# Optimization experiments

Measured on AMD Instinct MI355X. Metric: run time of the kernel, lower is better.

The kernel has to match this reference:

```python
import jax, jax.numpy as jnp
import numpy as np

NQ = 4          # number of qubits (hardcoded in the original module)
LET = 'pqrs'    # einsum letters for the 4 qubit axes


def setup_inputs() -> dict:
    key = jax.random.key(0)
    k1, k2 = jax.random.split(key)
    B = 1048576  # 2^20 samples
    x = jax.random.normal(k1, (B, NQ), dtype=jnp.float32)          # RX angles per sample
    weights = jax.random.normal(k2, (3, NQ, 3), dtype=jnp.float32) * 0.1  # (layers, wires, 3)
    return {"x": x, "weights": weights}


def _apply_1q(state, U, w):
    # state: (B,2,2,2,2) complex, U: (2,2) complex, applied on wire w
    sub = 'b' + LET
    out = sub.replace(LET[w], 'x')
    return jnp.einsum(f'x{LET[w]},{sub}->{out}', U, state)


def _cnot(state, c, t):
    # CNOT control c -> target t: flip target axis on the control=1 half
    s0, s1 = jnp.split(state, 2, axis=1 + c)
    s1 = jnp.flip(s1, axis=1 + t)
    return jnp.concatenate([s0, s1], axis=1 + c)


def _rot(phi, theta, omega):
    # PennyLane Rot(phi, theta, omega) = RZ(omega) RY(theta) RZ(phi)
    c = jnp.cos(theta * 0.5)
    s = jnp.sin(theta * 0.5)
    m00 = jnp.exp(-0.5j * (phi + omega)) * c
    m01 = -jnp.exp(0.5j * (phi - omega)) * s
    m10 = jnp.exp(-0.5j * (phi - omega)) * s
    m11 = jnp.exp(0.5j * (phi + omega)) * c
    return jnp.stack([jnp.stack([m00, m01]), jnp.stack([m10, m11])]).astype(jnp.complex64)


def _forward(x, weights):
    # --- RX(x_i) on |0>^4: product state, built as an outer product ---
    c = jnp.cos(x * 0.5)
    s = jnp.sin(x * 0.5)
    mi = np.complex64(-1j)
    vs = [jnp.stack([c[:, i].astype(jnp.complex64), mi * s[:, i]], axis=-1) for i in range(NQ)]
    state = jnp.einsum('bp,bq,br,bs->bpqrs', *vs)  # (B,2,2,2,2) complex64

    # --- StronglyEntanglingLayers (default ranges r = l % (NQ-1) + 1) ---
    n_layers = weights.shape[0]
    for l in range(n_layers):
        for i in range(NQ):
            U = _rot(weights[l, i, 0], weights[l, i, 1], weights[l, i, 2])
            state = _apply_1q(state, U, i)
        r = (l % (NQ - 1)) + 1
        for i in range(NQ):
            state = _cnot(state, i, (i + r) % NQ)

    # --- <Z_i> expectation values ---
    probs = state.real ** 2 + state.imag ** 2  # (B,2,2,2,2) float32
    outs = []
    for w in range(NQ):
        axes = tuple(a for a in range(1, NQ + 1) if a != w + 1)
        m = probs.sum(axis=axes)  # (B,2) marginal over wire w
        outs.append(m[:, 0] - m[:, 1])
    return jnp.stack(outs, axis=-1)  # (B, NQ)


def reference(x, weights):
    return _forward(x, weights)
```

## Files before the change

kernel.cpp:

```cpp
#include <hip/hip_runtime.h>
#include <hip/hip_bf16.h>


__global__ void build_V_kernel(const float* __restrict__ w, float* __restrict__ V) {
    int k = threadIdx.x;
    if (k >= 16) return;

    float ar[16], ai[16];
#pragma unroll
    for (int j = 0; j < 16; ++j) { ar[j] = (j == k) ? 1.f : 0.f; ai[j] = 0.f; }

#pragma unroll
    for (int l = 0; l < 3; ++l) {
#pragma unroll
        for (int i = 0; i < 4; ++i) {
            float phi = w[l * 12 + i * 3 + 0];
            float th  = w[l * 12 + i * 3 + 1];
            float om  = w[l * 12 + i * 3 + 2];
            float ct = cosf(0.5f * th), st = sinf(0.5f * th);
            float alpha = 0.5f * (phi + om), beta = 0.5f * (phi - om);
            float sa, ca, sb, cb;
            sincosf(alpha, &sa, &ca);
            sincosf(beta,  &sb, &cb);
            float m00r =  ca * ct, m00i = -sa * ct;
            float m01r = -cb * st, m01i = -sb * st;
            float m10r =  cb * st, m10i = -sb * st;
            float m11r =  ca * ct, m11i =  sa * ct;
            int mask = 1 << i;
#pragma unroll
            for (int j = 0; j < 16; ++j) {
                if (j & mask) continue;
                int j1 = j | mask;
                float a0r = ar[j],  a0i = ai[j];
                float a1r = ar[j1], a1i = ai[j1];
                ar[j]  = m00r * a0r - m00i * a0i + m01r * a1r - m01i * a1i;
                ai[j]  = m00r * a0i + m00i * a0r + m01r * a1i + m01i * a1r;
                ar[j1] = m10r * a0r - m10i * a0i + m11r * a1r - m11i * a1i;
                ai[j1] = m10r * a0i + m10i * a0r + m11r * a1i + m11i * a1r;
            }
        }
        int r = (l % 3) + 1;
#pragma unroll
        for (int i = 0; i < 4; ++i) {
            int c = i, t = (i + r) & 3;
            int cm = 1 << c, tm = 1 << t;
#pragma unroll
            for (int j = 0; j < 16; ++j) {
                if ((j & cm) && !(j & tm)) {
                    int j2 = j | tm;
                    float tr = ar[j], ti = ai[j];
                    ar[j] = ar[j2]; ai[j] = ai[j2];
                    ar[j2] = tr;    ai[j2] = ti;
                }
            }
        }
    }

    int p = __popc(k) & 3;
    float pr = (p == 0) ? 1.f : (p == 2) ? -1.f : 0.f;
    float pi = (p == 1) ? -1.f : (p == 3) ? 1.f : 0.f;
#pragma unroll
    for (int j = 0; j < 16; ++j) {
        float vr = ar[j] * pr - ai[j] * pi;
        float vi = ar[j] * pi + ai[j] * pr;
        V[j * 32 + k]      = vr;
        V[j * 32 + 16 + k] = vi;
    }
}

#define SAMPLES_PER_THREAD 2
#define BLOCK 256

__launch_bounds__(BLOCK)
__global__ void qlayer_kernel(const float* __restrict__ x,
                              const float* __restrict__ Vg,
                              float* __restrict__ out, int B) {
    __shared__ float V[512];
    {
        int t = threadIdx.x;
        if (t < 128) ((float4*)V)[t] = ((const float4*)Vg)[t];
    }
    __syncthreads();

    int base = blockIdx.x * (BLOCK * SAMPLES_PER_THREAD) + threadIdx.x;

#pragma unroll
    for (int s = 0; s < SAMPLES_PER_THREAD; ++s) {
        int idx = base + s * BLOCK;
        if (idx < B) {
            float4 xv = ((const float4*)x)[idx];
            float c0, s0, c1, s1, c2, s2, c3, s3;
            __sincosf(0.5f * xv.x, &s0, &c0);
            __sincosf(0.5f * xv.y, &s1, &c1);
            __sincosf(0.5f * xv.z, &s2, &c2);
            __sincosf(0.5f * xv.w, &s3, &c3);

            float m[16];
            m[0] = c0; m[1] = s0;
            m[2] = m[0] * s1; m[3] = m[1] * s1;
            m[0] *= c1;       m[1] *= c1;
#pragma unroll
            for (int k = 0; k < 4; ++k) { m[4 + k] = m[k] * s2; m[k] *= c2; }
#pragma unroll
            for (int k = 0; k < 8; ++k) { m[8 + k] = m[k] * s3; m[k] *= c3; }

            float z0 = 0.f, z1 = 0.f, z2 = 0.f, z3 = 0.f;
#pragma unroll
            for (int j = 0; j < 16; ++j) {
                float re = 0.f, im = 0.f;
#pragma unroll
                for (int k = 0; k < 16; ++k) {
                    re = fmaf(V[j * 32 + k],      m[k], re);
                    im = fmaf(V[j * 32 + 16 + k], m[k], im);
                }
                float p = fmaf(re, re, im * im);
                z0 += (j & 1) ? -p : p;
                z1 += (j & 2) ? -p : p;
                z2 += (j & 4) ? -p : p;
                z3 += (j & 8) ? -p : p;
            }
            float4 o; o.x = z0; o.y = z1; o.z = z2; o.w = z3;
            ((float4*)out)[idx] = o;
        }
    }
}

extern "C" void kernel_launch(void* const* d_in, const int* in_sizes, int n_in,
                              void* d_out, int out_size, void* d_ws, size_t ws_size,
                              hipStream_t stream) {
    const float* x = (const float*)d_in[0];
    const float* w = (const float*)d_in[1];
    float* out = (float*)d_out;
    float* V = (float*)d_ws;

    int B = in_sizes[0] / 4;

    build_V_kernel<<<1, 64, 0, stream>>>(w, V);

    int samples_per_block = BLOCK * SAMPLES_PER_THREAD;
    int grid = (B + samples_per_block - 1) / samples_per_block;
    qlayer_kernel<<<grid, BLOCK, 0, stream>>>(x, V, out, B);
}
```

Measured before the change: 97.74 us.

## Read V matrix from global/scalar path and reuse each coefficient across four samples

Drops the shared-memory staging of the 16x16 complex V matrix and reads it straight from global memory. V indices are uniform across the wavefront, so these loads can go through scalar loads. The loop is reordered so each V element is loaded once and applied to four samples per thread, and a template removes bounds checks when B divides evenly. This cuts LDS traffic and load count per FMA, at the cost of more VGPRs (64 mask values plus accumulators), which may lower occupancy.

```diff
diff --git a/kernel.cpp b/kernel.cpp
--- a/kernel.cpp
+++ b/kernel.cpp
@@ -68,58 +68,73 @@
     }
 }
 
-#define SAMPLES_PER_THREAD 2
+#define SPT 4
 #define BLOCK 256
 
+template <bool GUARD>
 __launch_bounds__(BLOCK)
 __global__ void qlayer_kernel(const float* __restrict__ x,
-                              const float* __restrict__ Vg,
+                              const float* __restrict__ V,
                               float* __restrict__ out, int B) {
-    __shared__ float V[512];
-    {
-        int t = threadIdx.x;
-        if (t < 128) ((float4*)V)[t] = ((const float4*)Vg)[t];
-    }
-    __syncthreads();
+    const int base = blockIdx.x * (BLOCK * SPT) + threadIdx.x;
 
-    int base = blockIdx.x * (BLOCK * SAMPLES_PER_THREAD) + threadIdx.x;
+    float m[SPT][16];
+    float z[SPT][4];
 
 #pragma unroll
-    for (int s = 0; s < SAMPLES_PER_THREAD; ++s) {
+    for (int s = 0; s < SPT; ++s) {
         int idx = base + s * BLOCK;
-        if (idx < B) {
-            float4 xv = ((const float4*)x)[idx];
-            float c0, s0, c1, s1, c2, s2, c3, s3;
-            __sincosf(0.5f * xv.x, &s0, &c0);
-            __sincosf(0.5f * xv.y, &s1, &c1);
-            __sincosf(0.5f * xv.z, &s2, &c2);
-            __sincosf(0.5f * xv.w, &s3, &c3);
+        float4 xv;
+        if (!GUARD || idx < B) xv = ((const float4*)x)[idx];
+        else xv = make_float4(0.f, 0.f, 0.f, 0.f);
+        float c0, s0, c1, s1, c2, s2, c3, s3;
+        __sincosf(0.5f * xv.x, &s0, &c0);
+        __sincosf(0.5f * xv.y, &s1, &c1);
+        __sincosf(0.5f * xv.z, &s2, &c2);
+        __sincosf(0.5f * xv.w, &s3, &c3);
 
-            float m[16];
-            m[0] = c0; m[1] = s0;
-            m[2] = m[0] * s1; m[3] = m[1] * s1;
-            m[0] *= c1;       m[1] *= c1;
+        float* ms = m[s];
+        ms[0] = c0; ms[1] = s0;
+        ms[2] = ms[0] * s1; ms[3] = ms[1] * s1;
+        ms[0] *= c1;        ms[1] *= c1;
 #pragma unroll
-            for (int k = 0; k < 4; ++k) { m[4 + k] = m[k] * s2; m[k] *= c2; }
+        for (int k = 0; k < 4; ++k) { ms[4 + k] = ms[k] * s2; ms[k] *= c2; }
 #pragma unroll
-            for (int k = 0; k < 8; ++k) { m[8 + k] = m[k] * s3; m[k] *= c3; }
+        for (int k = 0; k < 8; ++k) { ms[8 + k] = ms[k] * s3; ms[k] *= c3; }
 
-            float z0 = 0.f, z1 = 0.f, z2 = 0.f, z3 = 0.f;
+        z[s][0] = z[s][1] = z[s][2] = z[s][3] = 0.f;
+    }
+
 #pragma unroll
-            for (int j = 0; j < 16; ++j) {
-                float re = 0.f, im = 0.f;
+    for (int j = 0; j < 16; ++j) {
+        float re[SPT], im[SPT];
 #pragma unroll
-                for (int k = 0; k < 16; ++k) {
-                    re = fmaf(V[j * 32 + k],      m[k], re);
-                    im = fmaf(V[j * 32 + 16 + k], m[k], im);
-                }
-                float p = fmaf(re, re, im * im);
-                z0 += (j & 1) ? -p : p;
-                z1 += (j & 2) ? -p : p;
-                z2 += (j & 4) ? -p : p;
-                z3 += (j & 8) ? -p : p;
+        for (int s = 0; s < SPT; ++s) { re[s] = 0.f; im[s] = 0.f; }
+#pragma unroll
+        for (int k = 0; k < 16; ++k) {
+            const float vr = V[j * 32 + k];
+            const float vi = V[j * 32 + 16 + k];
+#pragma unroll
+            for (int s = 0; s < SPT; ++s) {
+                re[s] = fmaf(vr, m[s][k], re[s]);
+                im[s] = fmaf(vi, m[s][k], im[s]);
             }
-            float4 o; o.x = z0; o.y = z1; o.z = z2; o.w = z3;
+        }
+#pragma unroll
+        for (int s = 0; s < SPT; ++s) {
+            float p = fmaf(re[s], re[s], im[s] * im[s]);
+            z[s][0] += (j & 1) ? -p : p;
+            z[s][1] += (j & 2) ? -p : p;
+            z[s][2] += (j & 4) ? -p : p;
+            z[s][3] += (j & 8) ? -p : p;
+        }
+    }
+
+#pragma unroll
+    for (int s = 0; s < SPT; ++s) {
+        int idx = base + s * BLOCK;
+        if (!GUARD || idx < B) {
+            float4 o; o.x = z[s][0]; o.y = z[s][1]; o.z = z[s][2]; o.w = z[s][3];
             ((float4*)out)[idx] = o;
         }
     }
@@ -137,7 +152,10 @@
 
     build_V_kernel<<<1, 64, 0, stream>>>(w, V);
 
-    int samples_per_block = BLOCK * SAMPLES_PER_THREAD;
-    int grid = (B + samples_per_block - 1) / samples_per_block;
-    qlayer_kernel<<<grid, BLOCK, 0, stream>>>(x, V, out, B);
+    const int spb = BLOCK * SPT;
+    if (B % spb == 0) {
+        qlayer_kernel<false><<<B / spb, BLOCK, 0, stream>>>(x, V, out, B);
+    } else {
+        qlayer_kernel<true><<<(B + spb - 1) / spb, BLOCK, 0, stream>>>(x, V, out, B);
+    }
 }
```

After: 99.18 us. No clear change (+1.5%).
